# Performance work log

Hardware: AMD Instinct MI355X
Metric: run time of the kernel (lower is better)

Reference implementation:

```python
import jax, jax.numpy as jnp
import numpy as np

KS = 3          # image feature patch kernel size
RATE = 2        # downsample rate; alpha patches use kernel RATE*2, stride RATE
PENALTY = -10000.0
EPS = 1e-4
BN_EPS = 1e-5


def _pad(x, k, s):
    # reflect 'same' padding as in GCAModule.pad
    l = (k - s + 1) // 2
    r = (k - s) // 2
    return jnp.pad(x, ((0, 0), (0, 0), (l, r), (l, r)), mode='reflect')


def _extract_patches(x, k, s):
    # replicates reflect-pad + F.unfold + reshape -> (n, L, c, k, k)
    x = _pad(x, k, s)
    n, c, H, W = x.shape
    oh = (H - k) // s + 1
    ow = (W - k) // s + 1
    cols = [x[:, :, di:di + s * (oh - 1) + 1:s, dj:dj + s * (ow - 1) + 1:s]
            for di in range(k) for dj in range(k)]
    p = jnp.stack(cols, axis=2).reshape(n, c, k, k, oh * ow)  # (n,c,k,k,L)
    return jnp.transpose(p, (0, 4, 1, 2, 3))                  # (n,L,c,k,k)


def _deconv(score, kern):
    # torch: F.conv_transpose2d(score[None], kern, stride=RATE, padding=1) / 4
    # score: (L,h,w); kern: (L, ac, 4, 4) in torch conv_transpose (I,O,kh,kw) layout
    k = jnp.transpose(jnp.flip(kern, axis=(2, 3)), (1, 0, 2, 3))  # -> OIHW
    out = jax.lax.conv_general_dilated(
        score[None], k, window_strides=(1, 1), padding=[(2, 2), (2, 2)],
        lhs_dilation=(RATE, RATE), dimension_numbers=('NCHW', 'OIHW', 'NCHW'))
    return out[0] / 4.0


def gca_forward(img_feat, alpha_feat, unknown, gconv_w, gconv_b, oconv_w,
                bn_gamma, bn_beta):
    n = img_feat.shape[0]
    # guidance 1x1 conv + nearest downsample by RATE
    g = jnp.einsum('nchw,oc->nohw', img_feat, gconv_w) + gconv_b[None, :, None, None]
    g = g[:, :, ::RATE, ::RATE]
    u = unknown[:, :, ::RATE, ::RATE]
    # process_unknown_mask: per-sample softmax scales
    um = u.mean(axis=(2, 3))                                    # (n,1)
    km = 1.0 - um
    unknown_scale = jnp.clip(jnp.sqrt(um / km), 0.1, 10.0)      # (n,1)
    known_scale = jnp.clip(jnp.sqrt(km / um), 0.1, 10.0)        # (n,1)
    h, w = g.shape[2], g.shape[3]
    L = h * w
    img_ps = _extract_patches(g, KS, 1)                         # (n,L,c,3,3)
    alpha_ps = _extract_patches(alpha_feat, RATE * 2, RATE)     # (n,L,ac,4,4)
    unk_ps = _extract_patches(u, KS, 1)[:, :, 0].mean(axis=(2, 3))  # (n,L)
    # l2-normalized image patch kernels
    norm = jnp.sqrt(jnp.sum(img_ps * img_ps, axis=(2, 3, 4), keepdims=True))
    img_ps_n = img_ps / jnp.maximum(norm, EPS)
    # similarity: conv of padded g with patch kernels == patches-at-p . kernel-q
    sim = jnp.einsum('npckl,nqckl->nqp', img_ps, img_ps_n)      # (n,L,L)
    is_unknown = (unk_ps > 0.0).astype(sim.dtype)               # (n,L)
    scale = unknown_scale * is_unknown + known_scale * (1.0 - is_unknown)
    out = sim * scale[:, :, None]
    idx = jnp.arange(L)
    out = out.at[:, idx, idx].add(PENALTY * unk_ps)             # self-corr penalty
    gca = jax.nn.softmax(out, axis=1).reshape(n, L, h, w)
    prop = jax.vmap(_deconv)(gca, alpha_ps)                     # (n,ac,2h,2w)
    # out_conv: 1x1 conv (no bias) + BatchNorm (training stats) + residual
    y = jnp.einsum('nchw,oc->nohw', prop, oconv_w)
    mu = y.mean(axis=(0, 2, 3), keepdims=True)
    var = y.var(axis=(0, 2, 3), keepdims=True)
    y = (y - mu) / jnp.sqrt(var + BN_EPS)
    y = y * bn_gamma[None, :, None, None] + bn_beta[None, :, None, None]
    return y + alpha_feat


def setup_inputs():
    key = jax.random.key(0)
    ks = jax.random.split(key, 8)
    N, C, AC, H, W = 4, 256, 128, 64, 64
    img_feat = jax.random.normal(ks[0], (N, C, H, W), jnp.float32)
    alpha_feat = jax.random.normal(ks[1], (N, AC, H, W), jnp.float32)
    unknown = jax.random.randint(ks[2], (N, 1, H, W), 0, 2).astype(jnp.float32)
    gconv_w = jax.random.normal(ks[3], (C // 2, C), jnp.float32) / np.float32(np.sqrt(C))
    gconv_b = jax.random.normal(ks[4], (C // 2,), jnp.float32) * 0.01
    oconv_w = jax.random.normal(ks[5], (AC, AC), jnp.float32) / np.float32(np.sqrt(AC))
    bn_gamma = 0.001 + jax.random.normal(ks[6], (AC,), jnp.float32) * 0.001
    bn_beta = jax.random.normal(ks[7], (AC,), jnp.float32) * 0.001
    return dict(img_feat=img_feat, alpha_feat=alpha_feat, unknown=unknown,
                gconv_w=gconv_w, gconv_b=gconv_b, oconv_w=oconv_w,
                bn_gamma=bn_gamma, bn_beta=bn_beta)


def reference(img_feat, alpha_feat, unknown, gconv_w, gconv_b, oconv_w,
              bn_gamma, bn_beta):
    return gca_forward(img_feat, alpha_feat, unknown, gconv_w, gconv_b,
                       oconv_w, bn_gamma, bn_beta)
```

## Files before the change

kernel.cpp:

```cpp
#include <hip/hip_runtime.h>

#define NN 4
#define CIN 256
#define CH 128
#define HH 64
#define hh 32
#define L 1024
#define NB 2048
#define PENALTY -10000.0f
#define EPS 1e-4f

typedef __bf16 bf16x8 __attribute__((ext_vector_type(8)));
typedef float f32x4 __attribute__((ext_vector_type(4)));
typedef __attribute__((address_space(3))) void lds_t;
typedef __attribute__((address_space(1))) const void gbl_t;

__device__ __forceinline__ int refl32(int t) { return t < 0 ? -t : (t > 31 ? 62 - t : t); }
__device__ __forceinline__ int refl64(int t) { return t < 0 ? -t : (t > 63 ? 126 - t : t); }
__device__ __forceinline__ int swz(int k, int row) { return k ^ (((row >> 1) & 3) << 3); }

__global__ void k_prep(const float* __restrict__ img, const float* __restrict__ gw,
                       const float* __restrict__ ow, const float* __restrict__ unknown,
                       const float* __restrict__ alpha,
                       __bf16* __restrict__ Xb, __bf16* __restrict__ gwb,
                       __bf16* __restrict__ owb, float* __restrict__ unk,
                       float* __restrict__ scales, __bf16* __restrict__ Bt,
                       float* __restrict__ stats) {
    __shared__ float sm[CIN * 33];
    int bid = blockIdx.x, t = threadIdx.x;
    if (bid < 512) {
        int n = bid >> 7, o = bid & 127;
        const float* ap = alpha + ((size_t)(n * CH + o) << 12);
#pragma unroll
        for (int j = 0; j < 4; ++j) {
            int fi = t + j * 256;
            int row = fi >> 4, c4 = fi & 15;
            float4 v = *(const float4*)(ap + fi * 4);
            float* d = sm + row * 65 + c4 * 4;
            d[0] = v.x; d[1] = v.y; d[2] = v.z; d[3] = v.w;
        }
        __syncthreads();
        __bf16* Bn = Bt + ((size_t)(n * NB) << 10);
#pragma unroll
        for (int gi = 0; gi < 8; ++gi) {
            int g = gi * 256 + t;
            int ab = g >> 7, qg = g & 127;
            int a = ab >> 2, bb = ab & 3;
            int q0 = qg * 8;
            int qi = q0 >> 5, qj0 = q0 & 31;
            int ti = refl64(2 * qi + a - 1);
            const float* r = sm + ti * 65;
            __bf16 v[8];
#pragma unroll
            for (int s = 0; s < 8; ++s) v[s] = (__bf16)r[refl64(2 * (qj0 + s) + bb - 1)];
            int j = ab * 128 + o;
            *(bf16x8*)(Bn + ((size_t)j << 10) + swz(q0, j)) = *(bf16x8*)v;
        }
    } else if (bid < 640) {
        int idx = bid - 512;
        int i = idx & 31, n = idx >> 5;
        for (int e = t; e < CIN * 32; e += 256) {
            int c = e >> 5, jj = e & 31;
            sm[c * 33 + jj] = img[(((size_t)n * CIN + c) * HH + 2 * i) * HH + 2 * jj];
        }
        __syncthreads();
#pragma unroll
        for (int j = 0; j < 32; ++j) {
            int np = (n << 10) + i * 32 + j;
            int cl = swz(t, np);
            Xb[(size_t)np * CIN + t] = (__bf16)sm[cl * 33 + j];
        }
    } else if (bid < 644) {
        int n = bid - 640;
        float* u = sm;
        float* red = sm + 1024;
        float part = 0.f;
#pragma unroll
        for (int c = 0; c < 4; ++c) {
            int idx = t + c * 256;
            int i = idx >> 5, j = idx & 31;
            float v = unknown[n * 4096 + (2 * i) * HH + 2 * j];
            u[idx] = v;
            part += v;
        }
        red[t] = part;
        __syncthreads();
        for (int s = 128; s > 0; s >>= 1) {
            if (t < s) red[t] += red[t + s];
            __syncthreads();
        }
        if (t == 0) {
            float um = red[0] / 1024.0f;
            float km = 1.0f - um;
            scales[n * 2] = fminf(fmaxf(sqrtf(um / km), 0.1f), 10.0f);
            scales[n * 2 + 1] = fminf(fmaxf(sqrtf(km / um), 0.1f), 10.0f);
        }
#pragma unroll
        for (int c = 0; c < 4; ++c) {
            int idx = t + c * 256;
            int i = idx >> 5, j = idx & 31;
            float sum = 0.f;
#pragma unroll
            for (int di = -1; di <= 1; ++di)
#pragma unroll
                for (int dj = -1; dj <= 1; ++dj)
                    sum += u[refl32(i + di) * 32 + refl32(j + dj)];
            unk[n * L + idx] = sum * (1.0f / 9.0f);
        }
    } else {
        if (bid == 644) stats[t] = 0.f;
        for (int e = (bid - 644) * 256 + t; e < 49152; e += 36 * 256) {
            if (e < 32768) {
                int o = e >> 8, m = e & 255;
                gwb[e] = (__bf16)gw[o * 256 + swz(m, o)];
            } else {
                int e2 = e - 32768;
                int j = e2 >> 7, m = e2 & 127;
                owb[e2] = (__bf16)ow[j * 128 + swz(m, j)];
            }
        }
    }
}

__global__ __launch_bounds__(256, 2) void k_gemm0(const __bf16* __restrict__ Xb,
                                                  const __bf16* __restrict__ gwb,
                                                  const float* __restrict__ gb,
                                                  __bf16* __restrict__ gbf) {
    __shared__ __align__(16) __bf16 As[128 * 32];
    __shared__ __align__(16) __bf16 Bs[128 * 32];
    int p0 = blockIdx.x * 128;
    int t = threadIdx.x, l = t & 63, w = t >> 6;
    int wr = w >> 1, wc = w & 1;
    f32x4 acc[4][4] = {};
    for (int k0 = 0; k0 < CIN; k0 += 32) {
#pragma unroll
        for (int i = 0; i < 2; ++i) {
            const __bf16* srcA = Xb + (size_t)(p0 + i * 64 + (t >> 2)) * CIN + k0 + (t & 3) * 8;
            __builtin_amdgcn_global_load_lds((gbl_t*)srcA, (lds_t*)(As + i * 2048 + t * 8), 16, 0, 0);
            const __bf16* srcB = gwb + (size_t)(i * 64 + (t >> 2)) * CIN + k0 + (t & 3) * 8;
            __builtin_amdgcn_global_load_lds((gbl_t*)srcB, (lds_t*)(Bs + i * 2048 + t * 8), 16, 0, 0);
        }
        __syncthreads();
        int gl = l >> 4, r = l & 15;
        bf16x8 av[4], bv[4];
#pragma unroll
        for (int m = 0; m < 4; ++m) {
            int row = wr * 64 + m * 16 + r;
            av[m] = *(const bf16x8*)(As + row * 32 + swz(gl << 3, row));
            int col = wc * 64 + m * 16 + r;
            bv[m] = *(const bf16x8*)(Bs + col * 32 + swz(gl << 3, col));
        }
#pragma unroll
        for (int m = 0; m < 4; ++m)
#pragma unroll
            for (int c2 = 0; c2 < 4; ++c2)
                acc[m][c2] = __builtin_amdgcn_mfma_f32_16x16x32_bf16(av[m], bv[c2], acc[m][c2], 0, 0, 0);
        __syncthreads();
    }
    int r = l & 15, hi = l >> 4;
#pragma unroll
    for (int m = 0; m < 4; ++m)
#pragma unroll
        for (int c2 = 0; c2 < 4; ++c2) {
            int o = wc * 64 + c2 * 16 + r;
            float bias = gb[o];
#pragma unroll
            for (int reg = 0; reg < 4; ++reg) {
                int row = p0 + wr * 64 + m * 16 + hi * 4 + reg;
                gbf[((size_t)row << 7) + o] = (__bf16)(acc[m][c2][reg] + bias);
            }
        }
}

__global__ void k_ssqf(const __bf16* __restrict__ gbf, const float* __restrict__ unk,
                       const float* __restrict__ scales, float* __restrict__ f) {
    __shared__ float ssqs[1024];
    int n = blockIdx.x, t = threadIdx.x;
    {
        const __bf16* rp = gbf + (((size_t)(n << 10) + t) << 7);
        float s = 0.f;
#pragma unroll
        for (int kk = 0; kk < 16; ++kk) {
            bf16x8 v = *(const bf16x8*)(rp + kk * 8);
#pragma unroll
            for (int u2 = 0; u2 < 8; ++u2) {
                float x = (float)v[u2];
                s += x * x;
            }
        }
        ssqs[t] = s;
    }
    __syncthreads();
    float us = scales[n * 2], ks = scales[n * 2 + 1];
    int pi = t >> 5, pj = t & 31;
    float sum = 0.f;
#pragma unroll
    for (int di = -1; di <= 1; ++di)
#pragma unroll
        for (int dj = -1; dj <= 1; ++dj)
            sum += ssqs[refl32(pi + di) * 32 + refl32(pj + dj)];
    float norm = sqrtf(sum);
    float sc = unk[n * L + t] > 0.f ? us : ks;
    f[n * L + t] = sc / fmaxf(norm, EPS);
}

__global__ __launch_bounds__(256, 1) void k_gemm1(const __bf16* __restrict__ gbf,
                                                  const float* __restrict__ f,
                                                  const float* __restrict__ unk,
                                                  float* __restrict__ W) {
    __shared__ __align__(16) __bf16 As[4 * 6144];
    __shared__ __align__(16) __bf16 Bs[4 * 6144];
    int n = blockIdx.z;
    int p0 = blockIdx.y * 128, q0 = blockIdx.x * 128;
    const __bf16* gn = gbf + ((size_t)n << 17);
    int t = threadIdx.x, l = t & 63, w = t >> 6;
    int wr = w >> 1, wc = w & 1;
    int by4 = blockIdx.y * 4, bx4 = blockIdx.x * 4;
    int rbA = by4 - 1; rbA = rbA < 0 ? 0 : (rbA > 26 ? 26 : rbA);
    int rbB = bx4 - 1; rbB = rbB < 0 ? 0 : (rbB > 26 ? 26 : rbB);
#pragma unroll
    for (int k = 0; k < 12; ++k) {
        int chunk = k / 3;
        int rem = (k % 3) * 256 + t;
        int wrow = rem >> 2, sg = rem & 3;
        int so = (chunk << 5) + ((sg ^ ((wrow >> 1) & 3)) << 3);
        int grA = ((rbA + (wrow >> 5)) << 5) + (wrow & 31);
        __builtin_amdgcn_global_load_lds((gbl_t*)(gn + (size_t)grA * 128 + so),
                                         (lds_t*)(As + chunk * 6144 + rem * 8), 16, 0, 0);
        int grB = ((rbB + (wrow >> 5)) << 5) + (wrow & 31);
        __builtin_amdgcn_global_load_lds((gbl_t*)(gn + (size_t)grB * 128 + so),
                                         (lds_t*)(Bs + chunk * 6144 + rem * 8), 16, 0, 0);
    }
    __syncthreads();
    int gl = l >> 4, r = l & 15;
    int rpA[4][3], cpA[4][3], rpB[4][3], cpB[4][3];
#pragma unroll
    for (int m = 0; m < 4; ++m) {
        int prow = wr * 64 + m * 16 + r;
        int qrow = wc * 64 + m * 16 + r;
#pragma unroll
        for (int d = 0; d < 3; ++d) {
            rpA[m][d] = (refl32(by4 + (prow >> 5) + d - 1) - rbA) << 10;
            int cp = refl32((prow & 31) + d - 1);
            cpA[m][d] = cp * 32 + ((gl ^ ((cp >> 1) & 3)) << 3);
            rpB[m][d] = (refl32(bx4 + (qrow >> 5) + d - 1) - rbB) << 10;
            int cq = refl32((qrow & 31) + d - 1);
            cpB[m][d] = cq * 32 + ((gl ^ ((cq >> 1) & 3)) << 3);
        }
    }
    f32x4 acc[4][4] = {};
#pragma unroll
    for (int dk = 0; dk < 3; ++dk)
#pragma unroll
        for (int dl = 0; dl < 3; ++dl)
#pragma unroll
            for (int cc = 0; cc < 4; ++cc) {
                bf16x8 av[4], bv[4];
#pragma unroll
                for (int m = 0; m < 4; ++m) {
                    av[m] = *(const bf16x8*)(As + cc * 6144 + rpA[m][dk] + cpA[m][dl]);
                    bv[m] = *(const bf16x8*)(Bs + cc * 6144 + rpB[m][dk] + cpB[m][dl]);
                }
#pragma unroll
                for (int m = 0; m < 4; ++m)
#pragma unroll
                    for (int c2 = 0; c2 < 4; ++c2)
                        acc[m][c2] = __builtin_amdgcn_mfma_f32_16x16x32_bf16(av[m], bv[c2], acc[m][c2], 0, 0, 0);
            }
    int hi = l >> 4;
#pragma unroll
    for (int m = 0; m < 4; ++m)
#pragma unroll
        for (int c2 = 0; c2 < 4; ++c2) {
            int q = q0 + wc * 64 + c2 * 16 + r;
            float fq = f[n * L + q];
#pragma unroll
            for (int reg = 0; reg < 4; ++reg) {
                int p = p0 + wr * 64 + m * 16 + hi * 4 + reg;
                float val = acc[m][c2][reg] * fq;
                if (p == q) val += PENALTY * unk[n * L + p];
                W[((size_t)n << 20) + ((size_t)p << 10) + q] = val;
            }
        }
}

__global__ void k_softmax(const float* __restrict__ W, __bf16* __restrict__ Wb) {
    __shared__ float red[8];
    int row = blockIdx.x;
    int p = row & (L - 1);
    const float* Wr = W + (size_t)row * 1024;
    __bf16* Wbr = Wb + (size_t)row * 1024;
    int t = threadIdx.x, wv = t >> 6;
    float v[4];
    float mx = -1e30f;
#pragma unroll
    for (int ll = 0; ll < 4; ++ll) {
        v[ll] = Wr[t + ll * 256];
        mx = fmaxf(mx, v[ll]);
    }
#pragma unroll
    for (int off = 32; off > 0; off >>= 1) mx = fmaxf(mx, __shfl_xor(mx, off));
    if ((t & 63) == 0) red[wv] = mx;
    __syncthreads();
    mx = fmaxf(fmaxf(red[0], red[1]), fmaxf(red[2], red[3]));
    float sum = 0.f;
#pragma unroll
    for (int ll = 0; ll < 4; ++ll) {
        v[ll] = __expf(v[ll] - mx);
        sum += v[ll];
    }
#pragma unroll
    for (int off = 32; off > 0; off >>= 1) sum += __shfl_xor(sum, off);
    if ((t & 63) == 0) red[4 + wv] = sum;
    __syncthreads();
    float inv = 1.0f / (red[4] + red[5] + red[6] + red[7]);
#pragma unroll
    for (int ll = 0; ll < 4; ++ll) Wbr[swz(t + ll * 256, p)] = (__bf16)(v[ll] * inv);
}

__global__ __launch_bounds__(256, 2) void k_gemm2(const __bf16* __restrict__ Wb,
                                                  const __bf16* __restrict__ Bt,
                                                  __bf16* __restrict__ Tb) {
    int bid = blockIdx.x;
    int xcd = bid & 7, idx = bid >> 3;
    int n = xcd >> 1;
    int p0 = ((xcd & 1) * 4 + (idx & 3)) * 128;
    int j0 = (idx >> 2) * 128;
    __shared__ __align__(16) __bf16 As[4][4096];
    __shared__ __align__(16) __bf16 Bs[4][4096];
    const __bf16* An = Wb + ((size_t)n << 20);
    const __bf16* Bn = Bt + ((size_t)n * NB << 10);
    int t = threadIdx.x, l = t & 63, w = t >> 6;
    int wr = w >> 1, wc = w & 1;
    int gl = l >> 4, r = l & 15;
    f32x4 acc[4][4] = {};

    auto stage = [&](int buf, int k0) {
#pragma unroll
        for (int i = 0; i < 2; ++i) {
            int row = (t >> 2) + i * 64;
            int sgo = (t & 3) * 8;
            const __bf16* srcA = An + ((size_t)(p0 + row) << 10) + k0 + sgo;
            __builtin_amdgcn_global_load_lds((gbl_t*)srcA, (lds_t*)(&As[buf][row * 32 + sgo]), 16, 0, 0);
            const __bf16* srcB = Bn + ((size_t)(j0 + row) << 10) + k0 + sgo;
            __builtin_amdgcn_global_load_lds((gbl_t*)srcB, (lds_t*)(&Bs[buf][row * 32 + sgo]), 16, 0, 0);
        }
    };
    auto compute = [&](int buf) {
        bf16x8 av[4], bv[4];
#pragma unroll
        for (int m = 0; m < 4; ++m) {
            int row = wr * 64 + m * 16 + r;
            av[m] = *(const bf16x8*)(&As[buf][row * 32 + ((gl ^ ((row >> 1) & 3)) << 3)]);
            int col = wc * 64 + m * 16 + r;
            bv[m] = *(const bf16x8*)(&Bs[buf][col * 32 + ((gl ^ ((col >> 1) & 3)) << 3)]);
        }
#pragma unroll
        for (int m = 0; m < 4; ++m)
#pragma unroll
            for (int c2 = 0; c2 < 4; ++c2)
                acc[m][c2] = __builtin_amdgcn_mfma_f32_16x16x32_bf16(av[m], bv[c2], acc[m][c2], 0, 0, 0);
    };

    stage(0, 0);
    stage(1, 32);
    for (int it = 0; it < 32; ++it) {
        int buf = it & 3;
        if (it + 2 < 32) stage((it + 2) & 3, (it + 2) * 32);
        if (it < 30)
            asm volatile("s_waitcnt vmcnt(8)\n\ts_barrier" ::: "memory");
        else if (it == 30)
            asm volatile("s_waitcnt vmcnt(4)\n\ts_barrier" ::: "memory");
        else
            asm volatile("s_waitcnt vmcnt(0)\n\ts_barrier" ::: "memory");
        compute(buf);
    }
    int hi = l >> 4;
#pragma unroll
    for (int m = 0; m < 4; ++m)
#pragma unroll
        for (int c2 = 0; c2 < 4; ++c2) {
            int j = j0 + wc * 64 + c2 * 16 + r;
#pragma unroll
            for (int reg = 0; reg < 4; ++reg) {
                int p = p0 + wr * 64 + m * 16 + hi * 4 + reg;
                Tb[((size_t)n * L + p) * NB + j] = (__bf16)acc[m][c2][reg];
            }
        }
}

__global__ void k_oconv(const __bf16* __restrict__ owb, const __bf16* __restrict__ Tb,
                        float* __restrict__ y2, float* __restrict__ stats) {
    __shared__ __align__(16) __bf16 As[4 * 4096];
    __shared__ __align__(16) __bf16 Bp[4 * 2048];
    int n = blockIdx.z;
    int x0 = blockIdx.x * 64;
    int t = threadIdx.x, l = t & 63, w = t >> 6;
    int wr = w >> 1, wc = w & 1;
    int gl = l >> 4, r = l & 15, hi = l >> 4;
#pragma unroll
    for (int c = 0; c < 4; ++c)
#pragma unroll
        for (int i = 0; i < 2; ++i) {
            int h = i * 256 + t;
            const __bf16* src = owb + (size_t)(h >> 2) * CH + c * 32 + (h & 3) * 8;
            __builtin_amdgcn_global_load_lds((gbl_t*)src, (lds_t*)(As + c * 4096 + h * 8), 16, 0, 0);
        }
    const __bf16* Tn = Tb + ((size_t)(n * L) << 11);
#pragma unroll
    for (int it = 0; it < 4; ++it) {
        int e2 = it * 256 + t;
        int og = e2 & 15, pl = e2 >> 4;
        int pix = x0 + pl;
        int x = pix & 63, y = pix >> 6;
        float acc8[8] = {};
        int ap = (y + 1) & 1, bp = (x + 1) & 1;
#pragma unroll
        for (int da = 0; da < 2; ++da) {
            int a = ap + 2 * da;
            int ny = y + 1 - a;
            if (ny < 0 || ny >= 64) continue;
            int py = ny >> 1;
#pragma unroll
            for (int db = 0; db < 2; ++db) {
                int bb = bp + 2 * db;
                int nx = x + 1 - bb;
                if (nx < 0 || nx >= 64) continue;
                int px = nx >> 1;
                bf16x8 v = *(const bf16x8*)(Tn + (((size_t)(py * hh + px)) << 11) + (a * 4 + bb) * 128 + og * 8);
#pragma unroll
                for (int u2 = 0; u2 < 8; ++u2) acc8[u2] += (float)v[u2];
            }
        }
        __bf16 rr[8];
#pragma unroll
        for (int u2 = 0; u2 < 8; ++u2) rr[u2] = (__bf16)(acc8[u2] * 0.25f);
        int key = (pix >> 1) & 3;
        int dgl = (og & 3) ^ key;
        *(bf16x8*)(Bp + (og >> 2) * 2048 + pl * 32 + dgl * 8) = *(bf16x8*)rr;
    }
    __syncthreads();
    f32x4 acc[4][2] = {};
#pragma unroll
    for (int c = 0; c < 4; ++c) {
        bf16x8 av[4], bv[2];
#pragma unroll
        for (int m = 0; m < 4; ++m) {
            int row = wr * 64 + m * 16 + r;
            av[m] = *(const bf16x8*)(As + c * 4096 + row * 32 + ((gl ^ ((row >> 1) & 3)) << 3));
        }
#pragma unroll
        for (int c2 = 0; c2 < 2; ++c2) {
            int col = wc * 32 + c2 * 16 + r;
            bv[c2] = *(const bf16x8*)(Bp + c * 2048 + col * 32 + ((gl ^ ((col >> 1) & 3)) << 3));
        }
#pragma unroll
        for (int m = 0; m < 4; ++m)
#pragma unroll
            for (int c2 = 0; c2 < 2; ++c2)
                acc[m][c2] = __builtin_amdgcn_mfma_f32_16x16x32_bf16(av[m], bv[c2], acc[m][c2], 0, 0, 0);
    }
#pragma unroll
    for (int m = 0; m < 4; ++m)
#pragma unroll
        for (int c2 = 0; c2 < 2; ++c2) {
            int pix = x0 + wc * 32 + c2 * 16 + r;
#pragma unroll
            for (int reg = 0; reg < 4; ++reg) {
                int j = wr * 64 + m * 16 + hi * 4 + reg;
                y2[(((size_t)n * CH + j) << 12) + pix] = acc[m][c2][reg];
            }
        }
    __syncthreads();
    float* partS = (float*)As;
    float* partS2 = partS + 256;
#pragma unroll
    for (int m = 0; m < 4; ++m)
#pragma unroll
        for (int reg = 0; reg < 4; ++reg) {
            float s = 0.f, s2 = 0.f;
#pragma unroll
            for (int c2 = 0; c2 < 2; ++c2) {
                float v = acc[m][c2][reg];
                s += v;
                s2 += v * v;
            }
#pragma unroll
            for (int off = 1; off < 16; off <<= 1) {
                s += __shfl_xor(s, off);
                s2 += __shfl_xor(s2, off);
            }
            if (r == 0) {
                int j = wr * 64 + m * 16 + hi * 4 + reg;
                partS[j * 2 + wc] = s;
                partS2[j * 2 + wc] = s2;
            }
        }
    __syncthreads();
    if (t < 128) {
        atomicAdd(&stats[t * 2], partS[t * 2] + partS[t * 2 + 1]);
        atomicAdd(&stats[t * 2 + 1], partS2[t * 2] + partS2[t * 2 + 1]);
    }
}

__global__ void k_final(const float* __restrict__ y2, const float* __restrict__ stats,
                        const float* __restrict__ gamma, const float* __restrict__ beta,
                        const float* __restrict__ alpha, float* __restrict__ out) {
    int e4 = blockIdx.x * 256 + threadIdx.x;
    int oc = (e4 >> 10) & 127;
    float s1 = stats[oc * 2], s2 = stats[oc * 2 + 1];
    float mu = s1 * (1.0f / 16384.0f);
    float var = s2 * (1.0f / 16384.0f) - mu * mu;
    float inv = rsqrtf(var + 1e-5f);
    float g = gamma[oc], b = beta[oc];
    float4 yv = ((const float4*)y2)[e4];
    float4 av = ((const float4*)alpha)[e4];
    float4 o;
    o.x = (yv.x - mu) * inv * g + b + av.x;
    o.y = (yv.y - mu) * inv * g + b + av.y;
    o.z = (yv.z - mu) * inv * g + b + av.z;
    o.w = (yv.w - mu) * inv * g + b + av.w;
    ((float4*)out)[e4] = o;
}

extern "C" void kernel_launch(void* const* d_in, const int* in_sizes, int n_in,
                              void* d_out, int out_size, void* d_ws, size_t ws_size,
                              hipStream_t stream) {
    const float* img = (const float*)d_in[0];
    const float* alpha = (const float*)d_in[1];
    const float* unknown = (const float*)d_in[2];
    const float* gw = (const float*)d_in[3];
    const float* gb = (const float*)d_in[4];
    const float* ow = (const float*)d_in[5];
    const float* gamma = (const float*)d_in[6];
    const float* beta = (const float*)d_in[7];
    float* out = (float*)d_out;
    float* ws = (float*)d_ws;

    __bf16* Xb = (__bf16*)(ws);
    __bf16* gwb = (__bf16*)(ws + 524288);
    __bf16* owb = (__bf16*)(ws + 540672);
    __bf16* gbf = (__bf16*)(ws + 548864);
    float* f = ws + 811008;
    float* unk = ws + 815104;
    float* scales = ws + 819200;
    float* stats = ws + 819264;
    float* W = ws + 819520;
    __bf16* Wb = (__bf16*)(ws + 5013824);
    __bf16* Bt = (__bf16*)(ws + 7110976);
    __bf16* Tb = (__bf16*)(ws + 11305280);
    float* y2 = ws + 15499584;

    k_prep<<<680, 256, 0, stream>>>(img, gw, ow, unknown, alpha, Xb, gwb, owb, unk, scales, Bt, stats);
    k_gemm0<<<32, 256, 0, stream>>>(Xb, gwb, gb, gbf);
    k_ssqf<<<4, 1024, 0, stream>>>(gbf, unk, scales, f);
    k_gemm1<<<dim3(8, 8, 4), 256, 0, stream>>>(gbf, f, unk, W);
    k_softmax<<<4096, 256, 0, stream>>>(W, Wb);
    k_gemm2<<<512, 256, 0, stream>>>(Wb, Bt, Tb);
    k_oconv<<<dim3(64, 1, 4), 256, 0, stream>>>(owb, Tb, y2, stats);
    k_final<<<2048, 256, 0, stream>>>(y2, stats, gamma, beta, alpha, out);
}
```

Before: 102.7 us.

## Fuse all stages into one cooperative persistent kernel with grid syncs

Replaces the eight separate kernel launches with a single cooperative megakernel that loops over virtual blocks per stage and separates stages with grid-wide syncs. Independent work is regrouped so the alpha patch transpose runs alongside the guidance GEMM. The aim is to remove per-launch overhead and inter-kernel gaps. In exchange it adds grid.sync costs, uses a large shared-memory footprint that may limit occupancy, and fixes the grid at 256 times occupancy blocks, which may underfill some stages.

```diff
diff --git a/kernel.cpp b/kernel.cpp
--- a/kernel.cpp
+++ b/kernel.cpp
@@ -1,4 +1,7 @@
 #include <hip/hip_runtime.h>
+#include <hip/hip_cooperative_groups.h>
+
+namespace cg = cooperative_groups;
 
 #define NN 4
 #define CIN 256
@@ -19,508 +22,542 @@
 __device__ __forceinline__ int refl64(int t) { return t < 0 ? -t : (t > 63 ? 126 - t : t); }
 __device__ __forceinline__ int swz(int k, int row) { return k ^ (((row >> 1) & 3) << 3); }
 
-__global__ void k_prep(const float* __restrict__ img, const float* __restrict__ gw,
-                       const float* __restrict__ ow, const float* __restrict__ unknown,
-                       const float* __restrict__ alpha,
-                       __bf16* __restrict__ Xb, __bf16* __restrict__ gwb,
-                       __bf16* __restrict__ owb, float* __restrict__ unk,
-                       float* __restrict__ scales, __bf16* __restrict__ Bt,
-                       float* __restrict__ stats) {
-    __shared__ float sm[CIN * 33];
-    int bid = blockIdx.x, t = threadIdx.x;
-    if (bid < 512) {
-        int n = bid >> 7, o = bid & 127;
-        const float* ap = alpha + ((size_t)(n * CH + o) << 12);
-#pragma unroll
-        for (int j = 0; j < 4; ++j) {
-            int fi = t + j * 256;
-            int row = fi >> 4, c4 = fi & 15;
-            float4 v = *(const float4*)(ap + fi * 4);
-            float* d = sm + row * 65 + c4 * 4;
-            d[0] = v.x; d[1] = v.y; d[2] = v.z; d[3] = v.w;
-        }
-        __syncthreads();
-        __bf16* Bn = Bt + ((size_t)(n * NB) << 10);
-#pragma unroll
-        for (int gi = 0; gi < 8; ++gi) {
-            int g = gi * 256 + t;
-            int ab = g >> 7, qg = g & 127;
-            int a = ab >> 2, bb = ab & 3;
-            int q0 = qg * 8;
-            int qi = q0 >> 5, qj0 = q0 & 31;
-            int ti = refl64(2 * qi + a - 1);
-            const float* r = sm + ti * 65;
-            __bf16 v[8];
-#pragma unroll
-            for (int s = 0; s < 8; ++s) v[s] = (__bf16)r[refl64(2 * (qj0 + s) + bb - 1)];
-            int j = ab * 128 + o;
-            *(bf16x8*)(Bn + ((size_t)j << 10) + swz(q0, j)) = *(bf16x8*)v;
-        }
-    } else if (bid < 640) {
-        int idx = bid - 512;
-        int i = idx & 31, n = idx >> 5;
-        for (int e = t; e < CIN * 32; e += 256) {
-            int c = e >> 5, jj = e & 31;
-            sm[c * 33 + jj] = img[(((size_t)n * CIN + c) * HH + 2 * i) * HH + 2 * jj];
-        }
-        __syncthreads();
-#pragma unroll
-        for (int j = 0; j < 32; ++j) {
-            int np = (n << 10) + i * 32 + j;
-            int cl = swz(t, np);
-            Xb[(size_t)np * CIN + t] = (__bf16)sm[cl * 33 + j];
-        }
-    } else if (bid < 644) {
-        int n = bid - 640;
-        float* u = sm;
-        float* red = sm + 1024;
-        float part = 0.f;
-#pragma unroll
-        for (int c = 0; c < 4; ++c) {
-            int idx = t + c * 256;
-            int i = idx >> 5, j = idx & 31;
-            float v = unknown[n * 4096 + (2 * i) * HH + 2 * j];
-            u[idx] = v;
-            part += v;
-        }
-        red[t] = part;
-        __syncthreads();
-        for (int s = 128; s > 0; s >>= 1) {
-            if (t < s) red[t] += red[t + s];
+extern "C" __global__ void __launch_bounds__(256, 2) mega(
+    const float* __restrict__ img, const float* __restrict__ alpha,
+    const float* __restrict__ unknown, const float* __restrict__ gw,
+    const float* __restrict__ gb, const float* __restrict__ ow,
+    const float* __restrict__ gamma, const float* __restrict__ beta,
+    float* __restrict__ out, float* ws) {
+    __shared__ __align__(16) unsigned char RAW[75008];
+    cg::grid_group grid = cg::this_grid();
+    const int bid = blockIdx.x, t = threadIdx.x;
+    const int GD = gridDim.x;
+
+    __bf16* Xb = (__bf16*)(ws);
+    __bf16* gwb = (__bf16*)(ws + 524288);
+    __bf16* owb = (__bf16*)(ws + 540672);
+    __bf16* gbf = (__bf16*)(ws + 548864);
+    float* unk = ws + 815104;
+    float* scales = ws + 819200;
+    float* stats = ws + 819264;
+    float* W = ws + 819520;
+    __bf16* Wb = (__bf16*)(ws + 5013824);
+    __bf16* Bt = (__bf16*)(ws + 7110976);
+    __bf16* Tb = (__bf16*)(ws + 11305280);
+    float* y2 = ws + 15499584;
+
+    for (int vb = bid; vb < 168; vb += GD) {
+        float* sm = (float*)RAW;
+        if (vb < 128) {
+            int i = vb & 31, n = vb >> 5;
+            for (int e = t; e < CIN * 32; e += 256) {
+                int c = e >> 5, jj = e & 31;
+                sm[c * 33 + jj] = img[(((size_t)n * CIN + c) * HH + 2 * i) * HH + 2 * jj];
+            }
             __syncthreads();
-        }
-        if (t == 0) {
-            float um = red[0] / 1024.0f;
-            float km = 1.0f - um;
-            scales[n * 2] = fminf(fmaxf(sqrtf(um / km), 0.1f), 10.0f);
-            scales[n * 2 + 1] = fminf(fmaxf(sqrtf(km / um), 0.1f), 10.0f);
-        }
-#pragma unroll
-        for (int c = 0; c < 4; ++c) {
-            int idx = t + c * 256;
-            int i = idx >> 5, j = idx & 31;
-            float sum = 0.f;
-#pragma unroll
-            for (int di = -1; di <= 1; ++di)
-#pragma unroll
-                for (int dj = -1; dj <= 1; ++dj)
-                    sum += u[refl32(i + di) * 32 + refl32(j + dj)];
-            unk[n * L + idx] = sum * (1.0f / 9.0f);
-        }
-    } else {
-        if (bid == 644) stats[t] = 0.f;
-        for (int e = (bid - 644) * 256 + t; e < 49152; e += 36 * 256) {
-            if (e < 32768) {
-                int o = e >> 8, m = e & 255;
-                gwb[e] = (__bf16)gw[o * 256 + swz(m, o)];
-            } else {
-                int e2 = e - 32768;
-                int j = e2 >> 7, m = e2 & 127;
-                owb[e2] = (__bf16)ow[j * 128 + swz(m, j)];
-            }
-        }
-    }
-}
-
-__global__ __launch_bounds__(256, 2) void k_gemm0(const __bf16* __restrict__ Xb,
-                                                  const __bf16* __restrict__ gwb,
-                                                  const float* __restrict__ gb,
-                                                  __bf16* __restrict__ gbf) {
-    __shared__ __align__(16) __bf16 As[128 * 32];
-    __shared__ __align__(16) __bf16 Bs[128 * 32];
-    int p0 = blockIdx.x * 128;
-    int t = threadIdx.x, l = t & 63, w = t >> 6;
-    int wr = w >> 1, wc = w & 1;
-    f32x4 acc[4][4] = {};
-    for (int k0 = 0; k0 < CIN; k0 += 32) {
-#pragma unroll
-        for (int i = 0; i < 2; ++i) {
-            const __bf16* srcA = Xb + (size_t)(p0 + i * 64 + (t >> 2)) * CIN + k0 + (t & 3) * 8;
-            __builtin_amdgcn_global_load_lds((gbl_t*)srcA, (lds_t*)(As + i * 2048 + t * 8), 16, 0, 0);
-            const __bf16* srcB = gwb + (size_t)(i * 64 + (t >> 2)) * CIN + k0 + (t & 3) * 8;
-            __builtin_amdgcn_global_load_lds((gbl_t*)srcB, (lds_t*)(Bs + i * 2048 + t * 8), 16, 0, 0);
-        }
-        __syncthreads();
-        int gl = l >> 4, r = l & 15;
-        bf16x8 av[4], bv[4];
-#pragma unroll
-        for (int m = 0; m < 4; ++m) {
-            int row = wr * 64 + m * 16 + r;
-            av[m] = *(const bf16x8*)(As + row * 32 + swz(gl << 3, row));
-            int col = wc * 64 + m * 16 + r;
-            bv[m] = *(const bf16x8*)(Bs + col * 32 + swz(gl << 3, col));
-        }
-#pragma unroll
-        for (int m = 0; m < 4; ++m)
-#pragma unroll
-            for (int c2 = 0; c2 < 4; ++c2)
-                acc[m][c2] = __builtin_amdgcn_mfma_f32_16x16x32_bf16(av[m], bv[c2], acc[m][c2], 0, 0, 0);
-        __syncthreads();
-    }
-    int r = l & 15, hi = l >> 4;
-#pragma unroll
-    for (int m = 0; m < 4; ++m)
-#pragma unroll
-        for (int c2 = 0; c2 < 4; ++c2) {
-            int o = wc * 64 + c2 * 16 + r;
-            float bias = gb[o];
-#pragma unroll
-            for (int reg = 0; reg < 4; ++reg) {
-                int row = p0 + wr * 64 + m * 16 + hi * 4 + reg;
-                gbf[((size_t)row << 7) + o] = (__bf16)(acc[m][c2][reg] + bias);
-            }
-        }
-}
-
-__global__ void k_ssqf(const __bf16* __restrict__ gbf, const float* __restrict__ unk,
-                       const float* __restrict__ scales, float* __restrict__ f) {
-    __shared__ float ssqs[1024];
-    int n = blockIdx.x, t = threadIdx.x;
-    {
-        const __bf16* rp = gbf + (((size_t)(n << 10) + t) << 7);
-        float s = 0.f;
-#pragma unroll
-        for (int kk = 0; kk < 16; ++kk) {
-            bf16x8 v = *(const bf16x8*)(rp + kk * 8);
-#pragma unroll
-            for (int u2 = 0; u2 < 8; ++u2) {
-                float x = (float)v[u2];
-                s += x * x;
-            }
-        }
-        ssqs[t] = s;
-    }
-    __syncthreads();
-    float us = scales[n * 2], ks = scales[n * 2 + 1];
-    int pi = t >> 5, pj = t & 31;
-    float sum = 0.f;
-#pragma unroll
-    for (int di = -1; di <= 1; ++di)
-#pragma unroll
-        for (int dj = -1; dj <= 1; ++dj)
-            sum += ssqs[refl32(pi + di) * 32 + refl32(pj + dj)];
-    float norm = sqrtf(sum);
-    float sc = unk[n * L + t] > 0.f ? us : ks;
-    f[n * L + t] = sc / fmaxf(norm, EPS);
-}
-
-__global__ __launch_bounds__(256, 1) void k_gemm1(const __bf16* __restrict__ gbf,
-                                                  const float* __restrict__ f,
-                                                  const float* __restrict__ unk,
-                                                  float* __restrict__ W) {
-    __shared__ __align__(16) __bf16 As[4 * 6144];
-    __shared__ __align__(16) __bf16 Bs[4 * 6144];
-    int n = blockIdx.z;
-    int p0 = blockIdx.y * 128, q0 = blockIdx.x * 128;
-    const __bf16* gn = gbf + ((size_t)n << 17);
-    int t = threadIdx.x, l = t & 63, w = t >> 6;
-    int wr = w >> 1, wc = w & 1;
-    int by4 = blockIdx.y * 4, bx4 = blockIdx.x * 4;
-    int rbA = by4 - 1; rbA = rbA < 0 ? 0 : (rbA > 26 ? 26 : rbA);
-    int rbB = bx4 - 1; rbB = rbB < 0 ? 0 : (rbB > 26 ? 26 : rbB);
-#pragma unroll
-    for (int k = 0; k < 12; ++k) {
-        int chunk = k / 3;
-        int rem = (k % 3) * 256 + t;
-        int wrow = rem >> 2, sg = rem & 3;
-        int so = (chunk << 5) + ((sg ^ ((wrow >> 1) & 3)) << 3);
-        int grA = ((rbA + (wrow >> 5)) << 5) + (wrow & 31);
-        __builtin_amdgcn_global_load_lds((gbl_t*)(gn + (size_t)grA * 128 + so),
-                                         (lds_t*)(As + chunk * 6144 + rem * 8), 16, 0, 0);
-        int grB = ((rbB + (wrow >> 5)) << 5) + (wrow & 31);
-        __builtin_amdgcn_global_load_lds((gbl_t*)(gn + (size_t)grB * 128 + so),
-                                         (lds_t*)(Bs + chunk * 6144 + rem * 8), 16, 0, 0);
-    }
-    __syncthreads();
-    int gl = l >> 4, r = l & 15;
-    int rpA[4][3], cpA[4][3], rpB[4][3], cpB[4][3];
-#pragma unroll
-    for (int m = 0; m < 4; ++m) {
-        int prow = wr * 64 + m * 16 + r;
-        int qrow = wc * 64 + m * 16 + r;
-#pragma unroll
-        for (int d = 0; d < 3; ++d) {
-            rpA[m][d] = (refl32(by4 + (prow >> 5) + d - 1) - rbA) << 10;
-            int cp = refl32((prow & 31) + d - 1);
-            cpA[m][d] = cp * 32 + ((gl ^ ((cp >> 1) & 3)) << 3);
-            rpB[m][d] = (refl32(bx4 + (qrow >> 5) + d - 1) - rbB) << 10;
-            int cq = refl32((qrow & 31) + d - 1);
-            cpB[m][d] = cq * 32 + ((gl ^ ((cq >> 1) & 3)) << 3);
-        }
-    }
-    f32x4 acc[4][4] = {};
-#pragma unroll
-    for (int dk = 0; dk < 3; ++dk)
-#pragma unroll
-        for (int dl = 0; dl < 3; ++dl)
-#pragma unroll
-            for (int cc = 0; cc < 4; ++cc) {
+#pragma unroll
+            for (int j = 0; j < 32; ++j) {
+                int np = (n << 10) + i * 32 + j;
+                Xb[(size_t)np * CIN + t] = (__bf16)sm[swz(t, np) * 33 + j];
+            }
+            __syncthreads();
+        } else if (vb < 132) {
+            int n = vb - 128;
+            float* u = sm;
+            float* red = sm + 1024;
+            float part = 0.f;
+#pragma unroll
+            for (int c = 0; c < 4; ++c) {
+                int idx = t + c * 256;
+                int i = idx >> 5, j = idx & 31;
+                float v = unknown[n * 4096 + (2 * i) * HH + 2 * j];
+                u[idx] = v;
+                part += v;
+            }
+            red[t] = part;
+            __syncthreads();
+            for (int s = 128; s > 0; s >>= 1) {
+                if (t < s) red[t] += red[t + s];
+                __syncthreads();
+            }
+            if (t == 0) {
+                float um = red[0] / 1024.0f;
+                float km = 1.0f - um;
+                scales[n * 2] = fminf(fmaxf(sqrtf(um / km), 0.1f), 10.0f);
+                scales[n * 2 + 1] = fminf(fmaxf(sqrtf(km / um), 0.1f), 10.0f);
+            }
+#pragma unroll
+            for (int c = 0; c < 4; ++c) {
+                int idx = t + c * 256;
+                int i = idx >> 5, j = idx & 31;
+                float sum = 0.f;
+#pragma unroll
+                for (int di = -1; di <= 1; ++di)
+#pragma unroll
+                    for (int dj = -1; dj <= 1; ++dj)
+                        sum += u[refl32(i + di) * 32 + refl32(j + dj)];
+                unk[n * L + idx] = sum * (1.0f / 9.0f);
+            }
+            __syncthreads();
+        } else {
+            if (vb == 132) stats[t] = 0.f;
+            for (int e = (vb - 132) * 256 + t; e < 49152; e += 36 * 256) {
+                if (e < 32768) {
+                    int o = e >> 8, m = e & 255;
+                    gwb[e] = (__bf16)gw[o * 256 + swz(m, o)];
+                } else {
+                    int e2 = e - 32768;
+                    int j = e2 >> 7, m = e2 & 127;
+                    owb[e2] = (__bf16)ow[j * 128 + swz(m, j)];
+                }
+            }
+        }
+    }
+    grid.sync();
+
+    for (int vb = bid; vb < 544; vb += GD) {
+        if (vb < 32) {
+            __bf16* As = (__bf16*)RAW;
+            __bf16* Bs = As + 4096;
+            int p0 = vb * 128;
+            int l = t & 63, w = t >> 6;
+            int wr = w >> 1, wc = w & 1;
+            f32x4 acc[4][4] = {};
+            for (int k0 = 0; k0 < CIN; k0 += 32) {
+#pragma unroll
+                for (int i = 0; i < 2; ++i) {
+                    const __bf16* srcA = Xb + (size_t)(p0 + i * 64 + (t >> 2)) * CIN + k0 + (t & 3) * 8;
+                    __builtin_amdgcn_global_load_lds((gbl_t*)srcA, (lds_t*)(As + i * 2048 + t * 8), 16, 0, 0);
+                    const __bf16* srcB = gwb + (size_t)(i * 64 + (t >> 2)) * CIN + k0 + (t & 3) * 8;
+                    __builtin_amdgcn_global_load_lds((gbl_t*)srcB, (lds_t*)(Bs + i * 2048 + t * 8), 16, 0, 0);
+                }
+                __syncthreads();
+                int gl = l >> 4, r = l & 15;
                 bf16x8 av[4], bv[4];
 #pragma unroll
                 for (int m = 0; m < 4; ++m) {
-                    av[m] = *(const bf16x8*)(As + cc * 6144 + rpA[m][dk] + cpA[m][dl]);
-                    bv[m] = *(const bf16x8*)(Bs + cc * 6144 + rpB[m][dk] + cpB[m][dl]);
+                    int row = wr * 64 + m * 16 + r;
+                    av[m] = *(const bf16x8*)(As + row * 32 + swz(gl << 3, row));
+                    int col = wc * 64 + m * 16 + r;
+                    bv[m] = *(const bf16x8*)(Bs + col * 32 + swz(gl << 3, col));
                 }
 #pragma unroll
                 for (int m = 0; m < 4; ++m)
 #pragma unroll
                     for (int c2 = 0; c2 < 4; ++c2)
                         acc[m][c2] = __builtin_amdgcn_mfma_f32_16x16x32_bf16(av[m], bv[c2], acc[m][c2], 0, 0, 0);
-            }
-    int hi = l >> 4;
-#pragma unroll
-    for (int m = 0; m < 4; ++m)
-#pragma unroll
-        for (int c2 = 0; c2 < 4; ++c2) {
-            int q = q0 + wc * 64 + c2 * 16 + r;
-            float fq = f[n * L + q];
+                __syncthreads();
+            }
+            int r = l & 15, hi = l >> 4;
+#pragma unroll
+            for (int m = 0; m < 4; ++m)
+#pragma unroll
+                for (int c2 = 0; c2 < 4; ++c2) {
+                    int o = wc * 64 + c2 * 16 + r;
+                    float bias = gb[o];
+#pragma unroll
+                    for (int reg = 0; reg < 4; ++reg) {
+                        int row = p0 + wr * 64 + m * 16 + hi * 4 + reg;
+                        gbf[((size_t)row << 7) + o] = (__bf16)(acc[m][c2][reg] + bias);
+                    }
+                }
+        } else {
+            float* sm = (float*)RAW;
+            int blk = vb - 32;
+            int n = blk >> 7, o = blk & 127;
+            const float* ap = alpha + ((size_t)(n * CH + o) << 12);
+#pragma unroll
+            for (int j = 0; j < 4; ++j) {
+                int fi = t + j * 256;
+                int row = fi >> 4, c4 = fi & 15;
+                float4 v = *(const float4*)(ap + fi * 4);
+                float* d = sm + row * 65 + c4 * 4;
+                d[0] = v.x; d[1] = v.y; d[2] = v.z; d[3] = v.w;
+            }
+            __syncthreads();
+            __bf16* Bn = Bt + ((size_t)(n * NB) << 10);
+#pragma unroll
+            for (int gi = 0; gi < 8; ++gi) {
+                int g = gi * 256 + t;
+                int ab = g >> 7, qg = g & 127;
+                int a = ab >> 2, bb = ab & 3;
+                int q0 = qg * 8;
+                int qi = q0 >> 5, qj0 = q0 & 31;
+                int ti = refl64(2 * qi + a - 1);
+                const float* r = sm + ti * 65;
+                __bf16 v[8];
+#pragma unroll
+                for (int s = 0; s < 8; ++s) v[s] = (__bf16)r[refl64(2 * (qj0 + s) + bb - 1)];
+                int j = ab * 128 + o;
+                *(bf16x8*)(Bn + ((size_t)j << 10) + swz(q0, j)) = *(bf16x8*)v;
+            }
+            __syncthreads();
+        }
+    }
+    grid.sync();
+
+    if (bid < 256) {
+        __bf16* As1 = (__bf16*)RAW;
+        __bf16* Bh = (__bf16*)(RAW + 49152);
+        float* ssq = (float*)(RAW + 73728);
+        float* ftile = ssq + 192;
+        int n = bid >> 6;
+        int p0 = ((bid >> 3) & 7) * 128, q0 = (bid & 7) * 128;
+        const __bf16* gn = gbf + ((size_t)n << 17);
+        int l = t & 63, w = t >> 6;
+        int wr = w >> 1, wc = w & 1;
+        int by4 = ((bid >> 3) & 7) * 4, bx4 = (bid & 7) * 4;
+        int rbA = by4 - 1; rbA = rbA < 0 ? 0 : (rbA > 26 ? 26 : rbA);
+        int rbB = bx4 - 1; rbB = rbB < 0 ? 0 : (rbB > 26 ? 26 : rbB);
+#pragma unroll
+        for (int k = 0; k < 12; ++k) {
+            int chunk = k / 3;
+            int rem = (k % 3) * 256 + t;
+            int wrow = rem >> 2, sg = rem & 3;
+            int so = (chunk << 5) + ((sg ^ ((wrow >> 1) & 3)) << 3);
+            int grA = ((rbA + (wrow >> 5)) << 5) + (wrow & 31);
+            __builtin_amdgcn_global_load_lds((gbl_t*)(gn + (size_t)grA * 128 + so),
+                                             (lds_t*)(As1 + chunk * 6144 + rem * 8), 16, 0, 0);
+        }
+        auto stageB = [&](int h) {
+#pragma unroll
+            for (int k = 0; k < 6; ++k) {
+                int cl = k / 3;
+                int cc = 2 * h + cl;
+                int rem = (k % 3) * 256 + t;
+                int wrow = rem >> 2, sg = rem & 3;
+                int so = (cc << 5) + ((sg ^ ((wrow >> 1) & 3)) << 3);
+                int grB = ((rbB + (wrow >> 5)) << 5) + (wrow & 31);
+                __builtin_amdgcn_global_load_lds((gbl_t*)(gn + (size_t)grB * 128 + so),
+                                                 (lds_t*)(Bh + cl * 6144 + rem * 8), 16, 0, 0);
+            }
+        };
+        stageB(0);
+        int gl = l >> 4, r = l & 15;
+        int rpA_[4][3], cpA_[4][3], rpB_[4][3], cpB_[4][3];
+#pragma unroll
+        for (int m = 0; m < 4; ++m) {
+            int prow = wr * 64 + m * 16 + r;
+            int qrow = wc * 64 + m * 16 + r;
+#pragma unroll
+            for (int d = 0; d < 3; ++d) {
+                rpA_[m][d] = (refl32(by4 + (prow >> 5) + d - 1) - rbA) << 10;
+                int cp = refl32((prow & 31) + d - 1);
+                cpA_[m][d] = cp * 32 + ((gl ^ ((cp >> 1) & 3)) << 3);
+                rpB_[m][d] = (refl32(bx4 + (qrow >> 5) + d - 1) - rbB) << 10;
+                int cq = refl32((qrow & 31) + d - 1);
+                cpB_[m][d] = cq * 32 + ((gl ^ ((cq >> 1) & 3)) << 3);
+            }
+        }
+        f32x4 acc[4][4] = {};
+        float ssqAcc = 0.f;
+        auto computeH = [&](int h) {
+#pragma unroll
+            for (int dk = 0; dk < 3; ++dk)
+#pragma unroll
+                for (int dl = 0; dl < 3; ++dl)
+#pragma unroll
+                    for (int c = 0; c < 2; ++c) {
+                        int cc = 2 * h + c;
+                        bf16x8 av[4], bv[4];
+#pragma unroll
+                        for (int m = 0; m < 4; ++m) {
+                            av[m] = *(const bf16x8*)(As1 + cc * 6144 + rpA_[m][dk] + cpA_[m][dl]);
+                            bv[m] = *(const bf16x8*)(Bh + c * 6144 + rpB_[m][dk] + cpB_[m][dl]);
+                        }
+#pragma unroll
+                        for (int m = 0; m < 4; ++m)
+#pragma unroll
+                            for (int c2 = 0; c2 < 4; ++c2)
+                                acc[m][c2] = __builtin_amdgcn_mfma_f32_16x16x32_bf16(av[m], bv[c2], acc[m][c2], 0, 0, 0);
+                    }
+            if (t < 192) {
+                int key = (t >> 1) & 3;
+#pragma unroll
+                for (int c = 0; c < 2; ++c)
+#pragma unroll
+                    for (int g = 0; g < 4; ++g) {
+                        bf16x8 v = *(const bf16x8*)(Bh + c * 6144 + t * 32 + ((g ^ key) << 3));
+#pragma unroll
+                        for (int u2 = 0; u2 < 8; ++u2) {
+                            float x = (float)v[u2];
+                            ssqAcc += x * x;
+                        }
+                    }
+            }
+        };
+        __syncthreads();
+        computeH(0);
+        __syncthreads();
+        stageB(1);
+        __syncthreads();
+        computeH(1);
+        if (t < 192) ssq[t] = ssqAcc;
+        __syncthreads();
+        if (t < 128) {
+            int q = q0 + t;
+            int qi = q >> 5, qj = q & 31;
+            float sum = 0.f;
+#pragma unroll
+            for (int di = -1; di <= 1; ++di)
+#pragma unroll
+                for (int dj = -1; dj <= 1; ++dj)
+                    sum += ssq[(refl32(qi + di) - rbB) * 32 + refl32(qj + dj)];
+            float sc = unk[n * L + q] > 0.f ? scales[n * 2] : scales[n * 2 + 1];
+            ftile[t] = sc / fmaxf(sqrtf(sum), EPS);
+        }
+        __syncthreads();
+        int hi = l >> 4;
+#pragma unroll
+        for (int m = 0; m < 4; ++m)
+#pragma unroll
+            for (int c2 = 0; c2 < 4; ++c2) {
+                int q = q0 + wc * 64 + c2 * 16 + r;
+                float fq = ftile[wc * 64 + c2 * 16 + r];
+#pragma unroll
+                for (int reg = 0; reg < 4; ++reg) {
+                    int p = p0 + wr * 64 + m * 16 + hi * 4 + reg;
+                    float val = acc[m][c2][reg] * fq;
+                    if (p == q) val += PENALTY * unk[n * L + p];
+                    W[((size_t)n << 20) + ((size_t)p << 10) + q] = val;
+                }
+            }
+    }
+    grid.sync();
+
+    {
+        int wv = t >> 6, lane = t & 63;
+        for (int row = bid * 4 + wv; row < 4096; row += GD * 4) {
+            const float* Wr = W + (size_t)row * 1024;
+            float v[16];
+            float mx = -1e30f;
+#pragma unroll
+            for (int k = 0; k < 16; ++k) {
+                v[k] = Wr[lane + k * 64];
+                mx = fmaxf(mx, v[k]);
+            }
+#pragma unroll
+            for (int off = 32; off > 0; off >>= 1) mx = fmaxf(mx, __shfl_xor(mx, off));
+            float sum = 0.f;
+#pragma unroll
+            for (int k = 0; k < 16; ++k) {
+                v[k] = __expf(v[k] - mx);
+                sum += v[k];
+            }
+#pragma unroll
+            for (int off = 32; off > 0; off >>= 1) sum += __shfl_xor(sum, off);
+            float inv = 1.0f / sum;
+            int p = row & (L - 1);
+            int key = ((p >> 1) & 3) << 3;
+            __bf16* Wbr = Wb + (size_t)row * 1024;
+#pragma unroll
+            for (int k = 0; k < 16; ++k) {
+                int idx = lane + k * 64;
+                Wbr[idx ^ key] = (__bf16)(v[k] * inv);
+            }
+        }
+    }
+    grid.sync();
+
+    for (int vb = bid; vb < 512; vb += GD) {
+        int xcd = vb & 7, idx = vb >> 3;
+        int n = xcd >> 1;
+        int p0 = ((xcd & 1) * 4 + (idx & 3)) * 128;
+        int j0 = (idx >> 2) * 128;
+        __bf16* As2 = (__bf16*)RAW;
+        __bf16* Bs2 = (__bf16*)(RAW + 32768);
+        const __bf16* An = Wb + ((size_t)n << 20);
+        const __bf16* Bn = Bt + ((size_t)n * NB << 10);
+        int l = t & 63, w = t >> 6;
+        int wr = w >> 1, wc = w & 1;
+        int gl = l >> 4, r = l & 15;
+        f32x4 acc[4][4] = {};
+        auto stage = [&](int buf, int k0) {
+#pragma unroll
+            for (int i = 0; i < 2; ++i) {
+                int row = (t >> 2) + i * 64;
+                int sgo = (t & 3) * 8;
+                const __bf16* srcA = An + ((size_t)(p0 + row) << 10) + k0 + sgo;
+                __builtin_amdgcn_global_load_lds((gbl_t*)srcA, (lds_t*)(As2 + buf * 4096 + row * 32 + sgo), 16, 0, 0);
+                const __bf16* srcB = Bn + ((size_t)(j0 + row) << 10) + k0 + sgo;
+                __builtin_amdgcn_global_load_lds((gbl_t*)srcB, (lds_t*)(Bs2 + buf * 4096 + row * 32 + sgo), 16, 0, 0);
+            }
+        };
+        auto compute = [&](int buf) {
+            bf16x8 av[4], bv[4];
+#pragma unroll
+            for (int m = 0; m < 4; ++m) {
+                int row = wr * 64 + m * 16 + r;
+                av[m] = *(const bf16x8*)(As2 + buf * 4096 + row * 32 + ((gl ^ ((row >> 1) & 3)) << 3));
+                int col = wc * 64 + m * 16 + r;
+                bv[m] = *(const bf16x8*)(Bs2 + buf * 4096 + col * 32 + ((gl ^ ((col >> 1) & 3)) << 3));
+            }
+#pragma unroll
+            for (int m = 0; m < 4; ++m)
+#pragma unroll
+                for (int c2 = 0; c2 < 4; ++c2)
+                    acc[m][c2] = __builtin_amdgcn_mfma_f32_16x16x32_bf16(av[m], bv[c2], acc[m][c2], 0, 0, 0);
+        };
+        stage(0, 0);
+        stage(1, 32);
+        for (int it = 0; it < 32; ++it) {
+            int buf = it & 3;
+            if (it + 2 < 32) stage((it + 2) & 3, (it + 2) * 32);
+            if (it < 30)
+                asm volatile("s_waitcnt vmcnt(8)\n\ts_barrier" ::: "memory");
+            else if (it == 30)
+                asm volatile("s_waitcnt vmcnt(4)\n\ts_barrier" ::: "memory");
+            else
+                asm volatile("s_waitcnt vmcnt(0)\n\ts_barrier" ::: "memory");
+            compute(buf);
+        }
+        int hi = l >> 4;
+#pragma unroll
+        for (int m = 0; m < 4; ++m)
+#pragma unroll
+            for (int c2 = 0; c2 < 4; ++c2) {
+                int j = j0 + wc * 64 + c2 * 16 + r;
+#pragma unroll
+                for (int reg = 0; reg < 4; ++reg) {
+                    int p = p0 + wr * 64 + m * 16 + hi * 4 + reg;
+                    Tb[((size_t)n * L + p) * NB + j] = (__bf16)acc[m][c2][reg];
+                }
+            }
+    }
+    grid.sync();
+
+    for (int vb = bid; vb < 256; vb += GD) {
+        __bf16* Ao = (__bf16*)RAW;
+        __bf16* Bp = (__bf16*)(RAW + 32768);
+        int n = vb >> 6;
+        int x0 = (vb & 63) * 64;
+        int l = t & 63, w = t >> 6;
+        int wr = w >> 1, wc = w & 1;
+        int gl = l >> 4, r = l & 15, hi = l >> 4;
+#pragma unroll
+        for (int c = 0; c < 4; ++c)
+#pragma unroll
+            for (int i = 0; i < 2; ++i) {
+                int h = i * 256 + t;
+                const __bf16* src = owb + (size_t)(h >> 2) * CH + c * 32 + (h & 3) * 8;
+                __builtin_amdgcn_global_load_lds((gbl_t*)src, (lds_t*)(Ao + c * 4096 + h * 8), 16, 0, 0);
+            }
+        const __bf16* Tn = Tb + ((size_t)(n * L) << 11);
+#pragma unroll
+        for (int it = 0; it < 4; ++it) {
+            int e2 = it * 256 + t;
+            int og = e2 & 15, pl = e2 >> 4;
+            int pix = x0 + pl;
+            int x = pix & 63, y = pix >> 6;
+            float acc8[8] = {};
+            int ap = (y + 1) & 1, bp = (x + 1) & 1;
+#pragma unroll
+            for (int da = 0; da < 2; ++da) {
+                int a = ap + 2 * da;
+                int ny = y + 1 - a;
+                if (ny < 0 || ny >= 64) continue;
+                int py = ny >> 1;
+#pragma unroll
+                for (int db = 0; db < 2; ++db) {
+                    int bb = bp + 2 * db;
+                    int nx = x + 1 - bb;
+                    if (nx < 0 || nx >= 64) continue;
+                    int px = nx >> 1;
+                    bf16x8 v = *(const bf16x8*)(Tn + (((size_t)(py * hh + px)) << 11) + (a * 4 + bb) * 128 + og * 8);
+#pragma unroll
+                    for (int u2 = 0; u2 < 8; ++u2) acc8[u2] += (float)v[u2];
+                }
+            }
+            __bf16 rr[8];
+#pragma unroll
+            for (int u2 = 0; u2 < 8; ++u2) rr[u2] = (__bf16)(acc8[u2] * 0.25f);
+            int key = (pix >> 1) & 3;
+            int dgl = (og & 3) ^ key;
+            *(bf16x8*)(Bp + (og >> 2) * 2048 + pl * 32 + dgl * 8) = *(bf16x8*)rr;
+        }
+        __syncthreads();
+        f32x4 acc[4][2] = {};
+#pragma unroll
+        for (int c = 0; c < 4; ++c) {
+            bf16x8 av[4], bv[2];
+#pragma unroll
+            for (int m = 0; m < 4; ++m) {
+                int row = wr * 64 + m * 16 + r;
+                av[m] = *(const bf16x8*)(Ao + c * 4096 + row * 32 + ((gl ^ ((row >> 1) & 3)) << 3));
+            }
+#pragma unroll
+            for (int c2 = 0; c2 < 2; ++c2) {
+                int col = wc * 32 + c2 * 16 + r;
+                bv[c2] = *(const bf16x8*)(Bp + c * 2048 + col * 32 + ((gl ^ ((col >> 1) & 3)) << 3));
+            }
+#pragma unroll
+            for (int m = 0; m < 4; ++m)
+#pragma unroll
+                for (int c2 = 0; c2 < 2; ++c2)
+                    acc[m][c2] = __builtin_amdgcn_mfma_f32_16x16x32_bf16(av[m], bv[c2], acc[m][c2], 0, 0, 0);
+        }
+#pragma unroll
+        for (int m = 0; m < 4; ++m)
+#pragma unroll
+            for (int c2 = 0; c2 < 2; ++c2) {
+                int pix = x0 + wc * 32 + c2 * 16 + r;
+#pragma unroll
+                for (int reg = 0; reg < 4; ++reg) {
+                    int j = wr * 64 + m * 16 + hi * 4 + reg;
+                    y2[(((size_t)n * CH + j) << 12) + pix] = acc[m][c2][reg];
+                }
+            }
+        __syncthreads();
+        float* partS = (float*)RAW;
+        float* partS2 = partS + 256;
+#pragma unroll
+        for (int m = 0; m < 4; ++m)
 #pragma unroll
             for (int reg = 0; reg < 4; ++reg) {
-                int p = p0 + wr * 64 + m * 16 + hi * 4 + reg;
-                float val = acc[m][c2][reg] * fq;
-                if (p == q) val += PENALTY * unk[n * L + p];
-                W[((size_t)n << 20) + ((size_t)p << 10) + q] = val;
-            }
-        }
-}
-
-__global__ void k_softmax(const float* __restrict__ W, __bf16* __restrict__ Wb) {
-    __shared__ float red[8];
-    int row = blockIdx.x;
-    int p = row & (L - 1);
-    const float* Wr = W + (size_t)row * 1024;
-    __bf16* Wbr = Wb + (size_t)row * 1024;
-    int t = threadIdx.x, wv = t >> 6;
-    float v[4];
-    float mx = -1e30f;
-#pragma unroll
-    for (int ll = 0; ll < 4; ++ll) {
-        v[ll] = Wr[t + ll * 256];
-        mx = fmaxf(mx, v[ll]);
-    }
-#pragma unroll
-    for (int off = 32; off > 0; off >>= 1) mx = fmaxf(mx, __shfl_xor(mx, off));
-    if ((t & 63) == 0) red[wv] = mx;
-    __syncthreads();
-    mx = fmaxf(fmaxf(red[0], red[1]), fmaxf(red[2], red[3]));
-    float sum = 0.f;
-#pragma unroll
-    for (int ll = 0; ll < 4; ++ll) {
-        v[ll] = __expf(v[ll] - mx);
-        sum += v[ll];
-    }
-#pragma unroll
-    for (int off = 32; off > 0; off >>= 1) sum += __shfl_xor(sum, off);
-    if ((t & 63) == 0) red[4 + wv] = sum;
-    __syncthreads();
-    float inv = 1.0f / (red[4] + red[5] + red[6] + red[7]);
-#pragma unroll
-    for (int ll = 0; ll < 4; ++ll) Wbr[swz(t + ll * 256, p)] = (__bf16)(v[ll] * inv);
-}
-
-__global__ __launch_bounds__(256, 2) void k_gemm2(const __bf16* __restrict__ Wb,
-                                                  const __bf16* __restrict__ Bt,
-                                                  __bf16* __restrict__ Tb) {
-    int bid = blockIdx.x;
-    int xcd = bid & 7, idx = bid >> 3;
-    int n = xcd >> 1;
-    int p0 = ((xcd & 1) * 4 + (idx & 3)) * 128;
-    int j0 = (idx >> 2) * 128;
-    __shared__ __align__(16) __bf16 As[4][4096];
-    __shared__ __align__(16) __bf16 Bs[4][4096];
-    const __bf16* An = Wb + ((size_t)n << 20);
-    const __bf16* Bn = Bt + ((size_t)n * NB << 10);
-    int t = threadIdx.x, l = t & 63, w = t >> 6;
-    int wr = w >> 1, wc = w & 1;
-    int gl = l >> 4, r = l & 15;
-    f32x4 acc[4][4] = {};
-
-    auto stage = [&](int buf, int k0) {
-#pragma unroll
-        for (int i = 0; i < 2; ++i) {
-            int row = (t >> 2) + i * 64;
-            int sgo = (t & 3) * 8;
-            const __bf16* srcA = An + ((size_t)(p0 + row) << 10) + k0 + sgo;
-            __builtin_amdgcn_global_load_lds((gbl_t*)srcA, (lds_t*)(&As[buf][row * 32 + sgo]), 16, 0, 0);
-            const __bf16* srcB = Bn + ((size_t)(j0 + row) << 10) + k0 + sgo;
-            __builtin_amdgcn_global_load_lds((gbl_t*)srcB, (lds_t*)(&Bs[buf][row * 32 + sgo]), 16, 0, 0);
-        }
-    };
-    auto compute = [&](int buf) {
-        bf16x8 av[4], bv[4];
-#pragma unroll
-        for (int m = 0; m < 4; ++m) {
-            int row = wr * 64 + m * 16 + r;
-            av[m] = *(const bf16x8*)(&As[buf][row * 32 + ((gl ^ ((row >> 1) & 3)) << 3)]);
-            int col = wc * 64 + m * 16 + r;
-            bv[m] = *(const bf16x8*)(&Bs[buf][col * 32 + ((gl ^ ((col >> 1) & 3)) << 3)]);
-        }
-#pragma unroll
-        for (int m = 0; m < 4; ++m)
-#pragma unroll
-            for (int c2 = 0; c2 < 4; ++c2)
-                acc[m][c2] = __builtin_amdgcn_mfma_f32_16x16x32_bf16(av[m], bv[c2], acc[m][c2], 0, 0, 0);
-    };
-
-    stage(0, 0);
-    stage(1, 32);
-    for (int it = 0; it < 32; ++it) {
-        int buf = it & 3;
-        if (it + 2 < 32) stage((it + 2) & 3, (it + 2) * 32);
-        if (it < 30)
-            asm volatile("s_waitcnt vmcnt(8)\n\ts_barrier" ::: "memory");
-        else if (it == 30)
-            asm volatile("s_waitcnt vmcnt(4)\n\ts_barrier" ::: "memory");
-        else
-            asm volatile("s_waitcnt vmcnt(0)\n\ts_barrier" ::: "memory");
-        compute(buf);
-    }
-    int hi = l >> 4;
-#pragma unroll
-    for (int m = 0; m < 4; ++m)
-#pragma unroll
-        for (int c2 = 0; c2 < 4; ++c2) {
-            int j = j0 + wc * 64 + c2 * 16 + r;
-#pragma unroll
-            for (int reg = 0; reg < 4; ++reg) {
-                int p = p0 + wr * 64 + m * 16 + hi * 4 + reg;
-                Tb[((size_t)n * L + p) * NB + j] = (__bf16)acc[m][c2][reg];
-            }
-        }
-}
-
-__global__ void k_oconv(const __bf16* __restrict__ owb, const __bf16* __restrict__ Tb,
-                        float* __restrict__ y2, float* __restrict__ stats) {
-    __shared__ __align__(16) __bf16 As[4 * 4096];
-    __shared__ __align__(16) __bf16 Bp[4 * 2048];
-    int n = blockIdx.z;
-    int x0 = blockIdx.x * 64;
-    int t = threadIdx.x, l = t & 63, w = t >> 6;
-    int wr = w >> 1, wc = w & 1;
-    int gl = l >> 4, r = l & 15, hi = l >> 4;
-#pragma unroll
-    for (int c = 0; c < 4; ++c)
-#pragma unroll
-        for (int i = 0; i < 2; ++i) {
-            int h = i * 256 + t;
-            const __bf16* src = owb + (size_t)(h >> 2) * CH + c * 32 + (h & 3) * 8;
-            __builtin_amdgcn_global_load_lds((gbl_t*)src, (lds_t*)(As + c * 4096 + h * 8), 16, 0, 0);
-        }
-    const __bf16* Tn = Tb + ((size_t)(n * L) << 11);
-#pragma unroll
-    for (int it = 0; it < 4; ++it) {
-        int e2 = it * 256 + t;
-        int og = e2 & 15, pl = e2 >> 4;
-        int pix = x0 + pl;
-        int x = pix & 63, y = pix >> 6;
-        float acc8[8] = {};
-        int ap = (y + 1) & 1, bp = (x + 1) & 1;
-#pragma unroll
-        for (int da = 0; da < 2; ++da) {
-            int a = ap + 2 * da;
-            int ny = y + 1 - a;
-            if (ny < 0 || ny >= 64) continue;
-            int py = ny >> 1;
-#pragma unroll
-            for (int db = 0; db < 2; ++db) {
-                int bb = bp + 2 * db;
-                int nx = x + 1 - bb;
-                if (nx < 0 || nx >= 64) continue;
-                int px = nx >> 1;
-                bf16x8 v = *(const bf16x8*)(Tn + (((size_t)(py * hh + px)) << 11) + (a * 4 + bb) * 128 + og * 8);
-#pragma unroll
-                for (int u2 = 0; u2 < 8; ++u2) acc8[u2] += (float)v[u2];
-            }
-        }
-        __bf16 rr[8];
-#pragma unroll
-        for (int u2 = 0; u2 < 8; ++u2) rr[u2] = (__bf16)(acc8[u2] * 0.25f);
-        int key = (pix >> 1) & 3;
-        int dgl = (og & 3) ^ key;
-        *(bf16x8*)(Bp + (og >> 2) * 2048 + pl * 32 + dgl * 8) = *(bf16x8*)rr;
-    }
-    __syncthreads();
-    f32x4 acc[4][2] = {};
-#pragma unroll
-    for (int c = 0; c < 4; ++c) {
-        bf16x8 av[4], bv[2];
-#pragma unroll
-        for (int m = 0; m < 4; ++m) {
-            int row = wr * 64 + m * 16 + r;
-            av[m] = *(const bf16x8*)(As + c * 4096 + row * 32 + ((gl ^ ((row >> 1) & 3)) << 3));
-        }
-#pragma unroll
-        for (int c2 = 0; c2 < 2; ++c2) {
-            int col = wc * 32 + c2 * 16 + r;
-            bv[c2] = *(const bf16x8*)(Bp + c * 2048 + col * 32 + ((gl ^ ((col >> 1) & 3)) << 3));
-        }
-#pragma unroll
-        for (int m = 0; m < 4; ++m)
-#pragma unroll
-            for (int c2 = 0; c2 < 2; ++c2)
-                acc[m][c2] = __builtin_amdgcn_mfma_f32_16x16x32_bf16(av[m], bv[c2], acc[m][c2], 0, 0, 0);
-    }
-#pragma unroll
-    for (int m = 0; m < 4; ++m)
-#pragma unroll
-        for (int c2 = 0; c2 < 2; ++c2) {
-            int pix = x0 + wc * 32 + c2 * 16 + r;
-#pragma unroll
-            for (int reg = 0; reg < 4; ++reg) {
-                int j = wr * 64 + m * 16 + hi * 4 + reg;
-                y2[(((size_t)n * CH + j) << 12) + pix] = acc[m][c2][reg];
-            }
-        }
-    __syncthreads();
-    float* partS = (float*)As;
-    float* partS2 = partS + 256;
-#pragma unroll
-    for (int m = 0; m < 4; ++m)
-#pragma unroll
-        for (int reg = 0; reg < 4; ++reg) {
-            float s = 0.f, s2 = 0.f;
-#pragma unroll
-            for (int c2 = 0; c2 < 2; ++c2) {
-                float v = acc[m][c2][reg];
-                s += v;
-                s2 += v * v;
-            }
-#pragma unroll
-            for (int off = 1; off < 16; off <<= 1) {
-                s += __shfl_xor(s, off);
-                s2 += __shfl_xor(s2, off);
-            }
-            if (r == 0) {
-                int j = wr * 64 + m * 16 + hi * 4 + reg;
-                partS[j * 2 + wc] = s;
-                partS2[j * 2 + wc] = s2;
-            }
-        }
-    __syncthreads();
-    if (t < 128) {
-        atomicAdd(&stats[t * 2], partS[t * 2] + partS[t * 2 + 1]);
-        atomicAdd(&stats[t * 2 + 1], partS2[t * 2] + partS2[t * 2 + 1]);
-    }
-}
-
-__global__ void k_final(const float* __restrict__ y2, const float* __restrict__ stats,
-                        const float* __restrict__ gamma, const float* __restrict__ beta,
-                        const float* __restrict__ alpha, float* __restrict__ out) {
-    int e4 = blockIdx.x * 256 + threadIdx.x;
-    int oc = (e4 >> 10) & 127;
-    float s1 = stats[oc * 2], s2 = stats[oc * 2 + 1];
-    float mu = s1 * (1.0f / 16384.0f);
-    float var = s2 * (1.0f / 16384.0f) - mu * mu;
-    float inv = rsqrtf(var + 1e-5f);
-    float g = gamma[oc], b = beta[oc];
-    float4 yv = ((const float4*)y2)[e4];
-    float4 av = ((const float4*)alpha)[e4];
-    float4 o;
-    o.x = (yv.x - mu) * inv * g + b + av.x;
-    o.y = (yv.y - mu) * inv * g + b + av.y;
-    o.z = (yv.z - mu) * inv * g + b + av.z;
-    o.w = (yv.w - mu) * inv * g + b + av.w;
-    ((float4*)out)[e4] = o;
+                float s = 0.f, s2 = 0.f;
+#pragma unroll
+                for (int c2 = 0; c2 < 2; ++c2) {
+                    float v = acc[m][c2][reg];
+                    s += v;
+                    s2 += v * v;
+                }
+#pragma unroll
+                for (int off = 1; off < 16; off <<= 1) {
+                    s += __shfl_xor(s, off);
+                    s2 += __shfl_xor(s2, off);
+                }
+                if (r == 0) {
+                    int j = wr * 64 + m * 16 + hi * 4 + reg;
+                    partS[j * 2 + wc] = s;
+                    partS2[j * 2 + wc] = s2;
+                }
+            }
+        __syncthreads();
+        if (t < 128) {
+            atomicAdd(&stats[t * 2], partS[t * 2] + partS[t * 2 + 1]);
+            atomicAdd(&stats[t * 2 + 1], partS2[t * 2] + partS2[t * 2 + 1]);
+        }
+        __syncthreads();
+    }
+    grid.sync();
+
+    for (int vb = bid; vb < 2048; vb += GD) {
+        int e4 = vb * 256 + t;
+        int oc = (e4 >> 10) & 127;
+        float s1 = stats[oc * 2], s2 = stats[oc * 2 + 1];
+        float mu = s1 * (1.0f / 16384.0f);
+        float var = s2 * (1.0f / 16384.0f) - mu * mu;
+        float inv = rsqrtf(var + 1e-5f);
+        float g = gamma[oc], b = beta[oc];
+        float4 yv = ((const float4*)y2)[e4];
+        float4 av = ((const float4*)alpha)[e4];
+        float4 o;
+        o.x = (yv.x - mu) * inv * g + b + av.x;
+        o.y = (yv.y - mu) * inv * g + b + av.y;
+        o.z = (yv.z - mu) * inv * g + b + av.z;
+        o.w = (yv.w - mu) * inv * g + b + av.w;
+        ((float4*)out)[e4] = o;
+    }
 }
 
 extern "C" void kernel_launch(void* const* d_in, const int* in_sizes, int n_in,
@@ -537,26 +574,15 @@
     float* out = (float*)d_out;
     float* ws = (float*)d_ws;
 
-    __bf16* Xb = (__bf16*)(ws);
-    __bf16* gwb = (__bf16*)(ws + 524288);
-    __bf16* owb = (__bf16*)(ws + 540672);
-    __bf16* gbf = (__bf16*)(ws + 548864);
-    float* f = ws + 811008;
-    float* unk = ws + 815104;
-    float* scales = ws + 819200;
-    float* stats = ws + 819264;
-    float* W = ws + 819520;
-    __bf16* Wb = (__bf16*)(ws + 5013824);
-    __bf16* Bt = (__bf16*)(ws + 7110976);
-    __bf16* Tb = (__bf16*)(ws + 11305280);
-    float* y2 = ws + 15499584;
-
-    k_prep<<<680, 256, 0, stream>>>(img, gw, ow, unknown, alpha, Xb, gwb, owb, unk, scales, Bt, stats);
-    k_gemm0<<<32, 256, 0, stream>>>(Xb, gwb, gb, gbf);
-    k_ssqf<<<4, 1024, 0, stream>>>(gbf, unk, scales, f);
-    k_gemm1<<<dim3(8, 8, 4), 256, 0, stream>>>(gbf, f, unk, W);
-    k_softmax<<<4096, 256, 0, stream>>>(W, Wb);
-    k_gemm2<<<512, 256, 0, stream>>>(Wb, Bt, Tb);
-    k_oconv<<<dim3(64, 1, 4), 256, 0, stream>>>(owb, Tb, y2, stats);
-    k_final<<<2048, 256, 0, stream>>>(y2, stats, gamma, beta, alpha, out);
+    static int nblk = 0;
+    if (nblk == 0) {
+        int occ = 0;
+        if (hipOccupancyMaxActiveBlocksPerMultiprocessor(&occ, (const void*)mega, 256, 0) != hipSuccess || occ < 1)
+            occ = 1;
+        if (occ > 2) occ = 2;
+        nblk = 256 * occ;
+    }
+    void* params[] = {(void*)&img, (void*)&alpha, (void*)&unknown, (void*)&gw, (void*)&gb,
+                      (void*)&ow, (void*)&gamma, (void*)&beta, (void*)&out, (void*)&ws};
+    hipLaunchCooperativeKernel((const void*)mega, dim3(nblk), dim3(256), params, 0, stream);
 }
```

Result: slower. 275.2 us (+168.0%).
